# Kernel tuning notes

Measured on AMD Instinct MI355X. Metric: run time of the kernel, lower is better.

Reference implementation:

```python
import jax, jax.numpy as jnp
import numpy as np

N, E, NF, EF = 50000, 1600000, 16, 8
H, HEADS, HD, L = 128, 4, 32, 3
EPS = 1e-5
NEG_SLOPE = 0.2


def layer_norm(x, g, b):
    mu = jnp.mean(x, axis=-1, keepdims=True)
    var = jnp.mean((x - mu) ** 2, axis=-1, keepdims=True)
    return g * (x - mu) * jax.lax.rsqrt(var + EPS) + b


def setup_inputs() -> dict:
    key = jax.random.key(0)
    ks = jax.random.split(key, 16)
    s = 0.02
    return {
        "x": jax.random.normal(ks[0], (N, NF), jnp.float32),
        "edge_index": jax.random.randint(ks[1], (2, E), 0, N, jnp.int32),
        "edge_attr": jax.random.normal(ks[2], (E, EF), jnp.float32),
        "Wn": jax.random.normal(ks[3], (NF, H), jnp.float32) * s,
        "bn": jnp.zeros((H,), jnp.float32),
        "We": jax.random.normal(ks[4], (EF, H), jnp.float32) * s,
        "be": jnp.zeros((H,), jnp.float32),
        "ln_g": jnp.ones((L, H), jnp.float32),
        "ln_b": jnp.zeros((L, H), jnp.float32),
        "Wg": jax.random.normal(ks[5], (L, H, HEADS * HD), jnp.float32) * s,
        "att_s": jax.random.normal(ks[6], (L, HEADS, HD), jnp.float32) * s,
        "att_d": jax.random.normal(ks[7], (L, HEADS, HD), jnp.float32) * s,
        "att_e": jax.random.normal(ks[8], (L, HEADS, HD), jnp.float32) * s,
        "W_edge": jax.random.normal(ks[9], (L, H, HEADS * HD), jnp.float32) * s,
        "bg": jnp.zeros((L, HEADS * HD), jnp.float32),
    }


def reference(x, edge_index, edge_attr, Wn, bn, We, be, ln_g, ln_b, Wg, att_s, att_d, att_e, W_edge, bg):
    n = x.shape[0]
    h = x @ Wn + bn                      # [N, H] node embedding
    e = edge_attr @ We + be              # [E, H] edge embedding
    src, dst = edge_index[0], edge_index[1]
    # PyG add_self_loops(fill_value='mean'): self-loop attr = mean of incoming edge attrs
    cnt = jax.ops.segment_sum(jnp.ones((e.shape[0],), e.dtype), dst, num_segments=n)
    loop_attr = jax.ops.segment_sum(e, dst, num_segments=n) / jnp.maximum(cnt, 1.0)[:, None]
    ar = jnp.arange(n, dtype=src.dtype)
    src_f = jnp.concatenate([src, ar])   # [E+N]
    dst_f = jnp.concatenate([dst, ar])
    e_f = jnp.concatenate([e, loop_attr], axis=0)  # [E+N, H]
    for i in range(Wg.shape[0]):
        x_in = layer_norm(h, ln_g[i], ln_b[i])               # pre-norm
        xs = (x_in @ Wg[i]).reshape(n, HEADS, HD)            # [N, heads, hd]
        ep = (e_f @ W_edge[i]).reshape(-1, HEADS, HD)        # [E+N, heads, hd]
        a_src = jnp.sum(xs * att_s[i], axis=-1)              # [N, heads]
        a_dst = jnp.sum(xs * att_d[i], axis=-1)
        a_edge = jnp.sum(ep * att_e[i], axis=-1)             # [E+N, heads]
        alpha = jax.nn.leaky_relu(a_src[src_f] + a_dst[dst_f] + a_edge, NEG_SLOPE)
        # scatter-softmax over edges sharing a destination node
        alpha = alpha - jax.ops.segment_max(alpha, dst_f, num_segments=n)[dst_f]
        ex = jnp.exp(alpha)
        w = ex / jax.ops.segment_sum(ex, dst_f, num_segments=n)[dst_f]  # [E+N, heads]
        msg = w[:, :, None] * xs[src_f]                      # [E+N, heads, hd]
        out = jax.ops.segment_sum(msg, dst_f, num_segments=n).reshape(n, HEADS * HD) + bg[i]
        h = h + jax.nn.relu(out)                             # proj is Identity; dropout eval-mode
    graph_emb = jnp.mean(h, axis=0, keepdims=True)           # batch=None path
    return h, graph_emb
```

## Files before the change

### kernel.cpp

```cpp
#include <hip/hip_runtime.h>

#define NN 50000
#define EE 1600000
#define HC 128
#define EPSV 1e-5f
#define NEGS 0.2f

#define NB_H0 6250
#define NB_HIST 6250
#define NB_PREP 230

typedef __bf16 bf16x8 __attribute__((ext_vector_type(8)));
typedef __bf16 bf16x2 __attribute__((ext_vector_type(2)));
typedef float f32x4 __attribute__((ext_vector_type(4)));

static inline int cdiv(int a, int b) { return (a + b - 1) / b; }

__device__ inline float blo(unsigned v) { return __uint_as_float(v << 16); }
__device__ inline float bhi(unsigned v) { return __uint_as_float(v & 0xffff0000u); }
__device__ inline unsigned pkbf(float a, float b) {
  bf16x2 p;
  p.x = (__bf16)a;
  p.y = (__bf16)b;
  return *reinterpret_cast<unsigned*>(&p);
}

__global__ __launch_bounds__(256) void k_pre(const float* __restrict__ x, const float* __restrict__ Wn,
                                             const float* __restrict__ bn, const float* __restrict__ lng,
                                             const float* __restrict__ lnb, float* __restrict__ h,
                                             __bf16* __restrict__ xln, const int* __restrict__ ei,
                                             int* __restrict__ cnt, const float* __restrict__ We,
                                             const float* __restrict__ be, const float* __restrict__ Wed,
                                             const float* __restrict__ atte, float* __restrict__ Pc,
                                             const float* __restrict__ Wg, const float* __restrict__ atts,
                                             const float* __restrict__ attd, __bf16* __restrict__ wgt,
                                             int nb_hist) {
  int b = blockIdx.x;
  int t = threadIdx.x;
  if (b < NB_H0) {
    int idx = b * 256 + t;
    int n = idx >> 5, c4 = (idx & 31) * 4;
    float4 acc = *(const float4*)(bn + c4);
    const float* xr = x + (size_t)n * 16;
#pragma unroll
    for (int f = 0; f < 16; ++f) {
      float xv = xr[f];
      float4 wv = *(const float4*)(Wn + (size_t)f * HC + c4);
      acc.x += xv * wv.x;
      acc.y += xv * wv.y;
      acc.z += xv * wv.z;
      acc.w += xv * wv.w;
    }
    *(float4*)(h + (size_t)n * HC + c4) = acc;
    float s = acc.x + acc.y + acc.z + acc.w;
    float sq = acc.x * acc.x + acc.y * acc.y + acc.z * acc.z + acc.w * acc.w;
#pragma unroll
    for (int m = 1; m < 32; m <<= 1) {
      s += __shfl_xor(s, m);
      sq += __shfl_xor(sq, m);
    }
    float mu = s * (1.f / 128.f);
    float var = sq * (1.f / 128.f) - mu * mu;
    float rs = rsqrtf(fmaxf(var, 0.f) + EPSV);
    float4 g = *(const float4*)(lng + c4);
    float4 bb = *(const float4*)(lnb + c4);
    uint2 o;
    o.x = pkbf((acc.x - mu) * rs * g.x + bb.x, (acc.y - mu) * rs * g.y + bb.y);
    o.y = pkbf((acc.z - mu) * rs * g.z + bb.z, (acc.w - mu) * rs * g.w + bb.w);
    *(uint2*)(xln + (size_t)n * HC + c4) = o;
  } else if (b < NB_H0 + nb_hist) {
    int e = (b - NB_H0) * 256 + t;
    if (e < EE) atomicAdd(&cnt[ei[EE + e]], 1);
  } else if (b == NB_H0 + nb_hist) {
    __shared__ float v[128][4];
    for (int i = 0; i < 3; ++i) {
      if (t < 128) {
#pragma unroll
        for (int hh = 0; hh < 4; ++hh) {
          float s = 0.f;
          for (int hd = 0; hd < 32; ++hd)
            s += Wed[((size_t)i * 128 + t) * 128 + hh * 32 + hd] * atte[i * 128 + hh * 32 + hd];
          v[t][hh] = s;
        }
      }
      __syncthreads();
      if (t < 32) {
        int f = t >> 2, hh = t & 3;
        float s = 0.f;
        for (int c2 = 0; c2 < 128; ++c2) s += We[f * 128 + c2] * v[c2][hh];
        Pc[i * 36 + f * 4 + hh] = s;
      }
      if (t < 4) {
        float s = 0.f;
        for (int c2 = 0; c2 < 128; ++c2) s += be[c2] * v[c2][t];
        Pc[i * 36 + 32 + t] = s;
      }
      __syncthreads();
    }
  } else {
    int idx = (b - NB_H0 - nb_hist - 1) * 256 + t;
    if (idx >= 3 * 144 * 136) return;
    int i = idx / (144 * 136);
    int rem = idx - i * (144 * 136);
    int n = rem / 136, kp = rem - n * 136;
    float v = 0.f;
    if (kp < 128) {
      if (n < 128) {
        v = Wg[(size_t)i * 16384 + kp * 128 + n];
      } else if (n < 136) {
        int hh = (n - 128) & 3;
        const float* av = ((n < 132) ? atts : attd) + i * 128 + hh * 32;
        const float* wr = Wg + (size_t)i * 16384 + kp * 128 + hh * 32;
        float s = 0.f;
#pragma unroll
        for (int j = 0; j < 32; ++j) s += wr[j] * av[j];
        v = s;
      }
    }
    wgt[idx] = (__bf16)v;
  }
}

__global__ __launch_bounds__(1024) void k_scan1(const int* __restrict__ cnt, int* __restrict__ tmp,
                                                int* __restrict__ bsum) {
  __shared__ int lds[1024];
  int t = threadIdx.x;
  int i = blockIdx.x * 1024 + t;
  int v = (i < NN) ? cnt[i] : 0;
  lds[t] = v;
  __syncthreads();
  for (int off = 1; off < 1024; off <<= 1) {
    int u = (t >= off) ? lds[t - off] : 0;
    __syncthreads();
    lds[t] += u;
    __syncthreads();
  }
  if (i < NN) tmp[i] = lds[t] - v;
  if (t == 1023) bsum[blockIdx.x] = lds[1023];
}

__global__ void k_scan2(int* bsum, int nb) {
  if (threadIdx.x == 0 && blockIdx.x == 0) {
    int run = 0;
    for (int b = 0; b < nb; ++b) { int q = bsum[b]; bsum[b] = run; run += q; }
  }
}

__global__ __launch_bounds__(1024) void k_scan3(const int* __restrict__ tmp, const int* __restrict__ bsum,
                                                int* __restrict__ row_ptr, int* __restrict__ wr_ptr) {
  int t = threadIdx.x;
  int i = blockIdx.x * 1024 + t;
  if (i < NN) {
    int v = tmp[i] + bsum[blockIdx.x];
    row_ptr[i] = v;
    wr_ptr[i] = v;
  }
  if (i == 0) row_ptr[NN] = EE;
}

__global__ __launch_bounds__(256) void k_build(const int* __restrict__ ei, const float* __restrict__ ea,
                                               const float* __restrict__ Pc, int* __restrict__ cntr,
                                               uint4* __restrict__ rec, int cap) {
  __shared__ float P[108];
  if (threadIdx.x < 108) P[threadIdx.x] = Pc[threadIdx.x];
  __syncthreads();
  int e = blockIdx.x * 256 + threadIdx.x;
  if (e >= EE) return;
  int s = ei[e], d = ei[EE + e];
  const float* ar = ea + (size_t)e * 8;
  float4 q0 = *(const float4*)ar;
  float4 q1 = *(const float4*)(ar + 4);
  float a[8] = {q0.x, q0.y, q0.z, q0.w, q1.x, q1.y, q1.z, q1.w};
  float r[3][4];
#pragma unroll
  for (int i = 0; i < 3; ++i) {
    const float* p = P + i * 36;
#pragma unroll
    for (int hh = 0; hh < 4; ++hh) {
      float s2 = p[32 + hh];
#pragma unroll
      for (int f = 0; f < 8; ++f) s2 += a[f] * p[f * 4 + hh];
      r[i][hh] = s2;
    }
  }
  size_t idx;
  int pos = atomicAdd(&cntr[d], 1);
  if (cap == 0) {
    idx = (size_t)pos;
  } else {
    if (pos >= cap) return;
    idx = (size_t)d * cap + pos;
  }
  uint4 r0, r1;
  r0.x = (unsigned)s;
  r0.y = pkbf(r[0][0], r[0][1]);
  r0.z = pkbf(r[0][2], r[0][3]);
  r0.w = pkbf(r[1][0], r[1][1]);
  r1.x = pkbf(r[1][2], r[1][3]);
  r1.y = pkbf(r[2][0], r[2][1]);
  r1.z = pkbf(r[2][2], r[2][3]);
  r1.w = 0;
  uint4* rp = rec + idx * 2;
  rp[0] = r0;
  rp[1] = r1;
}

__global__ __launch_bounds__(256) void k_node(const __bf16* __restrict__ xln, const __bf16* __restrict__ wgt,
                                              __bf16* __restrict__ xsb, float* __restrict__ asrc,
                                              float* __restrict__ adst) {
  __shared__ __bf16 sA[128][136];
  __shared__ __bf16 sB[144][136];
  int t = threadIdx.x;
  int n0 = blockIdx.x * 128;
  {
    char* bd = (char*)&sB[0][0];
    const char* bs = (const char*)wgt;
    for (int off = t * 16; off < 144 * 136 * 2; off += 4096)
      *(uint4*)(bd + off) = *(const uint4*)(bs + off);
  }
  {
    uint4 z = make_uint4(0, 0, 0, 0);
#pragma unroll
    for (int u = t; u < 128 * 16; u += 256) {
      int row = u >> 4, ck = (u & 15) * 8;
      int n = n0 + row;
      uint4 v = (n < NN) ? *(const uint4*)(xln + (size_t)n * HC + ck) : z;
      *(uint4*)&sA[row][ck] = v;
    }
  }
  __syncthreads();
  int lane = t & 63;
  int c15 = lane & 15, g = lane >> 4;
  int m0w = (t >> 6) * 32;
  f32x4 acc[18];
#pragma unroll
  for (int i = 0; i < 18; ++i) acc[i] = (f32x4){0.f, 0.f, 0.f, 0.f};
#pragma unroll
  for (int ks = 0; ks < 4; ++ks) {
    bf16x8 a0 = *(const bf16x8*)&sA[m0w + c15][ks * 32 + g * 8];
    bf16x8 a1 = *(const bf16x8*)&sA[m0w + 16 + c15][ks * 32 + g * 8];
#pragma unroll
    for (int nt = 0; nt < 9; ++nt) {
      bf16x8 bv = *(const bf16x8*)&sB[nt * 16 + c15][ks * 32 + g * 8];
      acc[nt] = __builtin_amdgcn_mfma_f32_16x16x32_bf16(a0, bv, acc[nt], 0, 0, 0);
      acc[9 + nt] = __builtin_amdgcn_mfma_f32_16x16x32_bf16(a1, bv, acc[9 + nt], 0, 0, 0);
    }
  }
#pragma unroll
  for (int mt = 0; mt < 2; ++mt) {
    int nbase = n0 + m0w + mt * 16 + g * 4;
#pragma unroll
    for (int r = 0; r < 4; ++r) {
      int n = nbase + r;
      if (n < NN) {
        __bf16* op = xsb + (size_t)n * HC + c15;
#pragma unroll
        for (int nt = 0; nt < 8; ++nt) op[nt * 16] = (__bf16)acc[mt * 9 + nt][r];
        float av = acc[mt * 9 + 8][r];
        if (c15 < 4) asrc[(size_t)n * 4 + c15] = av;
        else if (c15 < 8) adst[(size_t)n * 4 + c15 - 4] = av;
      }
    }
  }
}

__global__ __launch_bounds__(256) void k_aggr(const int* __restrict__ row_ptr, const int* __restrict__ deg,
                                              int cap, const unsigned* __restrict__ recd, int loff,
                                              const __bf16* __restrict__ xsb, const float* __restrict__ asrc,
                                              const float* __restrict__ adst, const float* __restrict__ bgi,
                                              float* __restrict__ h, const float* __restrict__ lng2,
                                              const float* __restrict__ lnb2, __bf16* __restrict__ xln) {
  int wid = (blockIdx.x * 256 + threadIdx.x) >> 6;
  if (wid >= NN) return;
  int lane = threadIdx.x & 63;
  int ch0 = 2 * lane, head = lane >> 4;
  int um = lane & 7;
  int sbase = head << 4;
  int hs = head >> 1;
  int j0, j1;
  if (cap == 0) {
    j0 = row_ptr[wid];
    j1 = row_ptr[wid + 1];
  } else {
    j0 = wid * cap;
    int dg = deg[wid];
    if (dg > cap) dg = cap;
    j1 = j0 + dg;
  }
  float ad = adst[(size_t)wid * 4 + head];
  float acc0 = 0.f, acc1 = 0.f, dsum = 0.f, aes = 0.f;
  int nfull = (j1 - j0) >> 3;
  int j = j0 + nfull * 8;
  if (nfull > 0) {
    int ss[8], ssn[8];
#pragma unroll
    for (int u = 0; u < 8; ++u) ss[u] = (int)recd[(size_t)(j0 + u) * 8];
    for (int c = 0; c < nfull; ++c) {
      int jc = j0 + c * 8;
      if (c + 1 < nfull) {
#pragma unroll
        for (int u = 0; u < 8; ++u) ssn[u] = (int)recd[(size_t)(jc + 8 + u) * 8];
      } else {
#pragma unroll
        for (int u = 0; u < 8; ++u) ssn[u] = ss[u];
      }
      unsigned aw = recd[(size_t)(jc + um) * 8 + loff + hs];
      float av = (head & 1) ? bhi(aw) : blo(aw);
      float as = asrc[(size_t)ss[um] * 4 + head];
      unsigned xv[8];
#pragma unroll
      for (int u = 0; u < 8; ++u) xv[u] = *(const unsigned*)(xsb + (size_t)ss[u] * HC + ch0);
      float alpha = as + ad + av;
      alpha = alpha > 0.f ? alpha : NEGS * alpha;
      float em = __expf(alpha);
      aes += av;
#pragma unroll
      for (int u = 0; u < 8; ++u) {
        float e = __shfl(em, sbase + u);
        acc0 += e * blo(xv[u]);
        acc1 += e * bhi(xv[u]);
        dsum += e;
      }
#pragma unroll
      for (int u = 0; u < 8; ++u) ss[u] = ssn[u];
    }
  }
  aes += __shfl_xor(aes, 1);
  aes += __shfl_xor(aes, 2);
  aes += __shfl_xor(aes, 4);
  for (; j < j1; ++j) {
    const unsigned* rp = recd + (size_t)j * 8;
    int s0 = (int)rp[0];
    unsigned aw = rp[loff + hs];
    float v0 = (head & 1) ? bhi(aw) : blo(aw);
    float as0 = asrc[(size_t)s0 * 4 + head];
    unsigned x0 = *(const unsigned*)(xsb + (size_t)s0 * HC + ch0);
    float a0 = as0 + ad + v0;
    a0 = a0 > 0.f ? a0 : NEGS * a0;
    float e0 = __expf(a0);
    acc0 += e0 * blo(x0);
    acc1 += e0 * bhi(x0);
    dsum += e0;
    aes += v0;
  }
  int dg = j1 - j0;
  float aself = (dg > 0) ? aes / (float)dg : 0.f;
  float al = asrc[(size_t)wid * 4 + head] + ad + aself;
  al = al > 0.f ? al : NEGS * al;
  float exl = __expf(al);
  unsigned xv = *(const unsigned*)(xsb + (size_t)wid * HC + ch0);
  float inv = 1.f / (dsum + exl);
  float o0 = (acc0 + exl * blo(xv)) * inv;
  float o1 = (acc1 + exl * bhi(xv)) * inv;
  float* hp = h + (size_t)wid * HC;
  float n0v = hp[ch0] + fmaxf(0.f, o0 + bgi[ch0]);
  float n1v = hp[ch0 + 1] + fmaxf(0.f, o1 + bgi[ch0 + 1]);
  hp[ch0] = n0v;
  hp[ch0 + 1] = n1v;
  if (xln) {
    float s = n0v + n1v, sq = n0v * n0v + n1v * n1v;
#pragma unroll
    for (int m = 1; m < 64; m <<= 1) {
      s += __shfl_xor(s, m);
      sq += __shfl_xor(sq, m);
    }
    float mu = s * (1.f / 128.f);
    float var = sq * (1.f / 128.f) - mu * mu;
    float rs = rsqrtf(fmaxf(var, 0.f) + EPSV);
    unsigned p = pkbf((n0v - mu) * rs * lng2[ch0] + lnb2[ch0], (n1v - mu) * rs * lng2[ch0 + 1] + lnb2[ch0 + 1]);
    *(unsigned*)(xln + (size_t)wid * HC + ch0) = p;
  }
}

__global__ __launch_bounds__(256) void k_emb(const float* __restrict__ h, float* __restrict__ emb) {
  int t = blockIdx.x * 256 + threadIdx.x;
  int stride = gridDim.x * 256;
  float s = 0.f;
  for (int i = t; i < NN * HC; i += stride) s += h[i];
  __shared__ float red[256];
  red[threadIdx.x] = s;
  __syncthreads();
  if (threadIdx.x < 128) {
    float v2 = red[threadIdx.x] + red[threadIdx.x + 128];
    atomicAdd(&emb[threadIdx.x], v2 * (1.f / NN));
  }
}

extern "C" void kernel_launch(void* const* d_in, const int* in_sizes, int n_in, void* d_out, int out_size,
                              void* d_ws, size_t ws_size, hipStream_t stream) {
  (void)in_sizes; (void)n_in; (void)out_size;
  const float* x = (const float*)d_in[0];
  const int* ei = (const int*)d_in[1];
  const float* ea = (const float*)d_in[2];
  const float* Wn = (const float*)d_in[3];
  const float* bn = (const float*)d_in[4];
  const float* We = (const float*)d_in[5];
  const float* be = (const float*)d_in[6];
  const float* lng = (const float*)d_in[7];
  const float* lnb = (const float*)d_in[8];
  const float* Wg = (const float*)d_in[9];
  const float* atts = (const float*)d_in[10];
  const float* attd = (const float*)d_in[11];
  const float* atte = (const float*)d_in[12];
  const float* Wed = (const float*)d_in[13];
  const float* bg = (const float*)d_in[14];
  float* h = (float*)d_out;
  float* emb = h + (size_t)NN * HC;

  char* w = (char*)d_ws;
  size_t off = 0;
  auto alloc = [&](size_t bytes) {
    void* p = w + off;
    off = (off + bytes + 255) & ~(size_t)255;
    return p;
  };
  __bf16* xsb = (__bf16*)alloc((size_t)NN * HC * 2);
  __bf16* xln = (__bf16*)alloc((size_t)NN * HC * 2);
  float* asrc = (float*)alloc((size_t)NN * 4 * 4);
  float* adst = (float*)alloc((size_t)NN * 4 * 4);
  int* cnt = (int*)alloc((size_t)NN * 4);
  int* row_ptr = (int*)alloc((size_t)(NN + 1) * 4);
  int* wr_ptr = (int*)alloc((size_t)NN * 4);
  int* bsum = (int*)alloc(256);
  int* stmp = (int*)alloc((size_t)NN * 4);
  float* Pc = (float*)alloc(3 * 36 * 4);
  __bf16* wgt = (__bf16*)alloc((size_t)3 * 144 * 136 * 2);

  size_t avail = (ws_size > off + 4096) ? (ws_size - off - 4096) : 0;
  size_t capv = avail / ((size_t)NN * 32);
  int cap = 0;
  if (capv >= 72) cap = (capv > 96) ? 96 : (int)capv;
  uint4* rec = (uint4*)alloc(cap ? (size_t)NN * cap * 32 : (size_t)EE * 32);

  hipMemsetAsync(cnt, 0, (size_t)NN * 4, stream);
  hipMemsetAsync(emb, 0, HC * 4, stream);

  if (cap) {
    k_pre<<<NB_H0 + 1 + NB_PREP, 256, 0, stream>>>(x, Wn, bn, lng, lnb, h, xln, ei, cnt, We, be, Wed, atte,
                                                   Pc, Wg, atts, attd, wgt, 0);
    k_build<<<cdiv(EE, 256), 256, 0, stream>>>(ei, ea, Pc, cnt, rec, cap);
  } else {
    k_pre<<<NB_H0 + NB_HIST + 1 + NB_PREP, 256, 0, stream>>>(x, Wn, bn, lng, lnb, h, xln, ei, cnt, We, be,
                                                             Wed, atte, Pc, Wg, atts, attd, wgt, NB_HIST);
    int nb = cdiv(NN, 1024);
    k_scan1<<<nb, 1024, 0, stream>>>(cnt, stmp, bsum);
    k_scan2<<<1, 64, 0, stream>>>(bsum, nb);
    k_scan3<<<nb, 1024, 0, stream>>>(stmp, bsum, row_ptr, wr_ptr);
    k_build<<<cdiv(EE, 256), 256, 0, stream>>>(ei, ea, Pc, wr_ptr, rec, 0);
  }

  for (int i = 0; i < 3; ++i) {
    k_node<<<cdiv(NN, 128), 256, 0, stream>>>(xln, wgt + (size_t)i * 144 * 136, xsb, asrc, adst);
    const float* g2 = (i < 2) ? (lng + (i + 1) * HC) : nullptr;
    const float* b2 = (i < 2) ? (lnb + (i + 1) * HC) : nullptr;
    __bf16* xo = (i < 2) ? xln : nullptr;
    k_aggr<<<cdiv(NN, 4), 256, 0, stream>>>(row_ptr, cnt, cap, (const unsigned*)rec, 1 + 2 * i, xsb, asrc,
                                            adst, bg + i * HC, h, g2, b2, xo);
  }
  k_emb<<<512, 256, 0, stream>>>(h, emb);
}
```

Before: 433.0 us.

## Pack edge records to 16 bytes with FP8 logits and split wave across edges

Edge attention logits are now stored as software-encoded e4m3 bytes, so each edge record shrinks from 32 to 16 bytes. This halves the record traffic in the build and aggregation kernels and allows a larger per-node capacity for the same workspace. The aggregation wave is remapped so each lane handles 4 channels, with the two wave halves processing alternate edges and combining their partial sums at the end. The cost is lower precision on the edge logit term and half-idle lanes in the remainder loop and epilogue.

```diff
diff --git a/kernel.cpp b/kernel.cpp
--- a/kernel.cpp
+++ b/kernel.cpp
@@ -23,6 +23,19 @@
   p.x = (__bf16)a;
   p.y = (__bf16)b;
   return *reinterpret_cast<unsigned*>(&p);
+}
+
+__device__ inline float dec_e4m3(unsigned u) {
+  unsigned bits = ((u & 0x80u) << 24) | ((u & 0x7Fu) << 20);
+  return __uint_as_float(bits) * 0x1p120f;
+}
+__device__ inline unsigned enc_e4m3(float v) {
+  unsigned b = __float_as_uint(v * 0x1p-120f);
+  unsigned mag = (b & 0x7fffffffu) + 0x00080000u;
+  return ((b >> 24) & 0x80u) | ((mag >> 20) & 0x7Fu);
+}
+__device__ inline unsigned enc4_e4m3(const float* r) {
+  return enc_e4m3(r[0]) | (enc_e4m3(r[1]) << 8) | (enc_e4m3(r[2]) << 16) | (enc_e4m3(r[3]) << 24);
 }
 
 __global__ __launch_bounds__(256) void k_pre(const float* __restrict__ x, const float* __restrict__ Wn,
@@ -160,7 +173,7 @@
 
 __global__ __launch_bounds__(256) void k_build(const int* __restrict__ ei, const float* __restrict__ ea,
                                                const float* __restrict__ Pc, int* __restrict__ cntr,
-                                               uint4* __restrict__ rec, int cap) {
+                                               unsigned char* __restrict__ rec8, int cap) {
   __shared__ float P[108];
   if (threadIdx.x < 108) P[threadIdx.x] = Pc[threadIdx.x];
   __syncthreads();
@@ -191,18 +204,12 @@
     if (pos >= cap) return;
     idx = (size_t)d * cap + pos;
   }
-  uint4 r0, r1;
-  r0.x = (unsigned)s;
-  r0.y = pkbf(r[0][0], r[0][1]);
-  r0.z = pkbf(r[0][2], r[0][3]);
-  r0.w = pkbf(r[1][0], r[1][1]);
-  r1.x = pkbf(r[1][2], r[1][3]);
-  r1.y = pkbf(r[2][0], r[2][1]);
-  r1.z = pkbf(r[2][2], r[2][3]);
-  r1.w = 0;
-  uint4* rp = rec + idx * 2;
-  rp[0] = r0;
-  rp[1] = r1;
+  uint4 rr;
+  rr.x = (unsigned)s;
+  rr.y = enc4_e4m3(r[0]);
+  rr.z = enc4_e4m3(r[1]);
+  rr.w = enc4_e4m3(r[2]);
+  *(uint4*)(rec8 + idx * 16) = rr;
 }
 
 __global__ __launch_bounds__(256) void k_node(const __bf16* __restrict__ xln, const __bf16* __restrict__ wgt,
@@ -265,7 +272,7 @@
 }
 
 __global__ __launch_bounds__(256) void k_aggr(const int* __restrict__ row_ptr, const int* __restrict__ deg,
-                                              int cap, const unsigned* __restrict__ recd, int loff,
+                                              int cap, const unsigned char* __restrict__ rec8, int layer,
                                               const __bf16* __restrict__ xsb, const float* __restrict__ asrc,
                                               const float* __restrict__ adst, const float* __restrict__ bgi,
                                               float* __restrict__ h, const float* __restrict__ lng2,
@@ -273,10 +280,10 @@
   int wid = (blockIdx.x * 256 + threadIdx.x) >> 6;
   if (wid >= NN) return;
   int lane = threadIdx.x & 63;
-  int ch0 = 2 * lane, head = lane >> 4;
-  int um = lane & 7;
-  int sbase = head << 4;
-  int hs = head >> 1;
+  int q = lane & 31, half = lane >> 5;
+  int ch0 = 4 * q, headc = q >> 3;
+  int um = lane & 7, headS = lane >> 4;
+  int aoff = 4 + 4 * layer + headS;
   int j0, j1;
   if (cap == 0) {
     j0 = row_ptr[wid];
@@ -287,38 +294,52 @@
     if (dg > cap) dg = cap;
     j1 = j0 + dg;
   }
-  float ad = adst[(size_t)wid * 4 + head];
-  float acc0 = 0.f, acc1 = 0.f, dsum = 0.f, aes = 0.f;
+  float adS = adst[(size_t)wid * 4 + headS];
+  float a0 = 0.f, a1 = 0.f, a2 = 0.f, a3 = 0.f, dsum = 0.f, aes = 0.f;
   int nfull = (j1 - j0) >> 3;
   int j = j0 + nfull * 8;
   if (nfull > 0) {
     int ss[8], ssn[8];
 #pragma unroll
-    for (int u = 0; u < 8; ++u) ss[u] = (int)recd[(size_t)(j0 + u) * 8];
+    for (int u = 0; u < 8; ++u) ss[u] = *(const int*)(rec8 + (size_t)(j0 + u) * 16);
     for (int c = 0; c < nfull; ++c) {
       int jc = j0 + c * 8;
       if (c + 1 < nfull) {
 #pragma unroll
-        for (int u = 0; u < 8; ++u) ssn[u] = (int)recd[(size_t)(jc + 8 + u) * 8];
+        for (int u = 0; u < 8; ++u) ssn[u] = *(const int*)(rec8 + (size_t)(jc + 8 + u) * 16);
       } else {
 #pragma unroll
         for (int u = 0; u < 8; ++u) ssn[u] = ss[u];
       }
-      unsigned aw = recd[(size_t)(jc + um) * 8 + loff + hs];
-      float av = (head & 1) ? bhi(aw) : blo(aw);
-      float as = asrc[(size_t)ss[um] * 4 + head];
-      unsigned xv[8];
-#pragma unroll
-      for (int u = 0; u < 8; ++u) xv[u] = *(const unsigned*)(xsb + (size_t)ss[u] * HC + ch0);
-      float alpha = as + ad + av;
+      float av = dec_e4m3(rec8[(size_t)(jc + um) * 16 + aoff]);
+      float as = asrc[(size_t)ss[um] * 4 + headS];
+      uint2 g0 = *(const uint2*)(xsb + (size_t)ss[0 + half] * HC + ch0);
+      uint2 g1 = *(const uint2*)(xsb + (size_t)ss[2 + half] * HC + ch0);
+      uint2 g2 = *(const uint2*)(xsb + (size_t)ss[4 + half] * HC + ch0);
+      uint2 g3 = *(const uint2*)(xsb + (size_t)ss[6 + half] * HC + ch0);
+      float alpha = as + adS + av;
       alpha = alpha > 0.f ? alpha : NEGS * alpha;
       float em = __expf(alpha);
       aes += av;
-#pragma unroll
-      for (int u = 0; u < 8; ++u) {
-        float e = __shfl(em, sbase + u);
-        acc0 += e * blo(xv[u]);
-        acc1 += e * bhi(xv[u]);
+      int sb = headc << 4;
+      {
+        float e = __shfl(em, sb + 0 + half);
+        a0 += e * blo(g0.x); a1 += e * bhi(g0.x); a2 += e * blo(g0.y); a3 += e * bhi(g0.y);
+        dsum += e;
+      }
+      {
+        float e = __shfl(em, sb + 2 + half);
+        a0 += e * blo(g1.x); a1 += e * bhi(g1.x); a2 += e * blo(g1.y); a3 += e * bhi(g1.y);
+        dsum += e;
+      }
+      {
+        float e = __shfl(em, sb + 4 + half);
+        a0 += e * blo(g2.x); a1 += e * bhi(g2.x); a2 += e * blo(g2.y); a3 += e * bhi(g2.y);
+        dsum += e;
+      }
+      {
+        float e = __shfl(em, sb + 6 + half);
+        a0 += e * blo(g3.x); a1 += e * bhi(g3.x); a2 += e * blo(g3.y); a3 += e * bhi(g3.y);
         dsum += e;
       }
 #pragma unroll
@@ -329,46 +350,63 @@
   aes += __shfl_xor(aes, 2);
   aes += __shfl_xor(aes, 4);
   for (; j < j1; ++j) {
-    const unsigned* rp = recd + (size_t)j * 8;
-    int s0 = (int)rp[0];
-    unsigned aw = rp[loff + hs];
-    float v0 = (head & 1) ? bhi(aw) : blo(aw);
-    float as0 = asrc[(size_t)s0 * 4 + head];
-    unsigned x0 = *(const unsigned*)(xsb + (size_t)s0 * HC + ch0);
-    float a0 = as0 + ad + v0;
-    a0 = a0 > 0.f ? a0 : NEGS * a0;
-    float e0 = __expf(a0);
-    acc0 += e0 * blo(x0);
-    acc1 += e0 * bhi(x0);
-    dsum += e0;
-    aes += v0;
-  }
+    int s0 = *(const int*)(rec8 + (size_t)j * 16);
+    float v0s = dec_e4m3(rec8[(size_t)j * 16 + aoff]);
+    float as0 = asrc[(size_t)s0 * 4 + headS];
+    float al0 = as0 + adS + v0s;
+    al0 = al0 > 0.f ? al0 : NEGS * al0;
+    float e0 = __expf(al0);
+    aes += v0s;
+    float ec = __shfl(e0, headc << 4);
+    if (half == 0) {
+      uint2 g = *(const uint2*)(xsb + (size_t)s0 * HC + ch0);
+      a0 += ec * blo(g.x); a1 += ec * bhi(g.x); a2 += ec * blo(g.y); a3 += ec * bhi(g.y);
+      dsum += ec;
+    }
+  }
+  a0 += __shfl_xor(a0, 32);
+  a1 += __shfl_xor(a1, 32);
+  a2 += __shfl_xor(a2, 32);
+  a3 += __shfl_xor(a3, 32);
+  dsum += __shfl_xor(dsum, 32);
+  float aesC = __shfl(aes, headc << 4);
   int dg = j1 - j0;
-  float aself = (dg > 0) ? aes / (float)dg : 0.f;
-  float al = asrc[(size_t)wid * 4 + head] + ad + aself;
+  float aself = (dg > 0) ? aesC / (float)dg : 0.f;
+  float al = asrc[(size_t)wid * 4 + headc] + adst[(size_t)wid * 4 + headc] + aself;
   al = al > 0.f ? al : NEGS * al;
   float exl = __expf(al);
-  unsigned xv = *(const unsigned*)(xsb + (size_t)wid * HC + ch0);
+  uint2 gs = *(const uint2*)(xsb + (size_t)wid * HC + ch0);
   float inv = 1.f / (dsum + exl);
-  float o0 = (acc0 + exl * blo(xv)) * inv;
-  float o1 = (acc1 + exl * bhi(xv)) * inv;
-  float* hp = h + (size_t)wid * HC;
-  float n0v = hp[ch0] + fmaxf(0.f, o0 + bgi[ch0]);
-  float n1v = hp[ch0 + 1] + fmaxf(0.f, o1 + bgi[ch0 + 1]);
-  hp[ch0] = n0v;
-  hp[ch0 + 1] = n1v;
-  if (xln) {
-    float s = n0v + n1v, sq = n0v * n0v + n1v * n1v;
-#pragma unroll
-    for (int m = 1; m < 64; m <<= 1) {
-      s += __shfl_xor(s, m);
-      sq += __shfl_xor(sq, m);
-    }
-    float mu = s * (1.f / 128.f);
-    float var = sq * (1.f / 128.f) - mu * mu;
-    float rs = rsqrtf(fmaxf(var, 0.f) + EPSV);
-    unsigned p = pkbf((n0v - mu) * rs * lng2[ch0] + lnb2[ch0], (n1v - mu) * rs * lng2[ch0 + 1] + lnb2[ch0 + 1]);
-    *(unsigned*)(xln + (size_t)wid * HC + ch0) = p;
+  float o0 = (a0 + exl * blo(gs.x)) * inv;
+  float o1 = (a1 + exl * bhi(gs.x)) * inv;
+  float o2 = (a2 + exl * blo(gs.y)) * inv;
+  float o3 = (a3 + exl * bhi(gs.y)) * inv;
+  if (half == 0) {
+    float4 hv = *(float4*)(h + (size_t)wid * HC + ch0);
+    float4 bgv = *(const float4*)(bgi + ch0);
+    float n0v = hv.x + fmaxf(0.f, o0 + bgv.x);
+    float n1v = hv.y + fmaxf(0.f, o1 + bgv.y);
+    float n2v = hv.z + fmaxf(0.f, o2 + bgv.z);
+    float n3v = hv.w + fmaxf(0.f, o3 + bgv.w);
+    *(float4*)(h + (size_t)wid * HC + ch0) = make_float4(n0v, n1v, n2v, n3v);
+    if (xln) {
+      float s = n0v + n1v + n2v + n3v;
+      float sq = n0v * n0v + n1v * n1v + n2v * n2v + n3v * n3v;
+#pragma unroll
+      for (int m = 1; m < 32; m <<= 1) {
+        s += __shfl_xor(s, m);
+        sq += __shfl_xor(sq, m);
+      }
+      float mu = s * (1.f / 128.f);
+      float var = sq * (1.f / 128.f) - mu * mu;
+      float rs = rsqrtf(fmaxf(var, 0.f) + EPSV);
+      float4 g = *(const float4*)(lng2 + ch0);
+      float4 b = *(const float4*)(lnb2 + ch0);
+      uint2 o;
+      o.x = pkbf((n0v - mu) * rs * g.x + b.x, (n1v - mu) * rs * g.y + b.y);
+      o.y = pkbf((n2v - mu) * rs * g.z + b.z, (n3v - mu) * rs * g.w + b.w);
+      *(uint2*)(xln + (size_t)wid * HC + ch0) = o;
+    }
   }
 }
 
@@ -427,10 +465,10 @@
   __bf16* wgt = (__bf16*)alloc((size_t)3 * 144 * 136 * 2);
 
   size_t avail = (ws_size > off + 4096) ? (ws_size - off - 4096) : 0;
-  size_t capv = avail / ((size_t)NN * 32);
+  size_t capv = avail / ((size_t)NN * 16);
   int cap = 0;
   if (capv >= 72) cap = (capv > 96) ? 96 : (int)capv;
-  uint4* rec = (uint4*)alloc(cap ? (size_t)NN * cap * 32 : (size_t)EE * 32);
+  unsigned char* rec8 = (unsigned char*)alloc(cap ? (size_t)NN * cap * 16 : (size_t)EE * 16);
 
   hipMemsetAsync(cnt, 0, (size_t)NN * 4, stream);
   hipMemsetAsync(emb, 0, HC * 4, stream);
@@ -438,7 +476,7 @@
   if (cap) {
     k_pre<<<NB_H0 + 1 + NB_PREP, 256, 0, stream>>>(x, Wn, bn, lng, lnb, h, xln, ei, cnt, We, be, Wed, atte,
                                                    Pc, Wg, atts, attd, wgt, 0);
-    k_build<<<cdiv(EE, 256), 256, 0, stream>>>(ei, ea, Pc, cnt, rec, cap);
+    k_build<<<cdiv(EE, 256), 256, 0, stream>>>(ei, ea, Pc, cnt, rec8, cap);
   } else {
     k_pre<<<NB_H0 + NB_HIST + 1 + NB_PREP, 256, 0, stream>>>(x, Wn, bn, lng, lnb, h, xln, ei, cnt, We, be,
                                                              Wed, atte, Pc, Wg, atts, attd, wgt, NB_HIST);
@@ -446,7 +484,7 @@
     k_scan1<<<nb, 1024, 0, stream>>>(cnt, stmp, bsum);
     k_scan2<<<1, 64, 0, stream>>>(bsum, nb);
     k_scan3<<<nb, 1024, 0, stream>>>(stmp, bsum, row_ptr, wr_ptr);
-    k_build<<<cdiv(EE, 256), 256, 0, stream>>>(ei, ea, Pc, wr_ptr, rec, 0);
+    k_build<<<cdiv(EE, 256), 256, 0, stream>>>(ei, ea, Pc, wr_ptr, rec8, 0);
   }
 
   for (int i = 0; i < 3; ++i) {
@@ -454,8 +492,8 @@
     const float* g2 = (i < 2) ? (lng + (i + 1) * HC) : nullptr;
     const float* b2 = (i < 2) ? (lnb + (i + 1) * HC) : nullptr;
     __bf16* xo = (i < 2) ? xln : nullptr;
-    k_aggr<<<cdiv(NN, 4), 256, 0, stream>>>(row_ptr, cnt, cap, (const unsigned*)rec, 1 + 2 * i, xsb, asrc,
-                                            adst, bg + i * HC, h, g2, b2, xo);
+    k_aggr<<<cdiv(NN, 4), 256, 0, stream>>>(row_ptr, cnt, cap, rec8, i, xsb, asrc, adst, bg + i * HC, h,
+                                            g2, b2, xo);
   }
   k_emb<<<512, 256, 0, stream>>>(h, emb);
 }
```

New measurement: 494.1 us. 1.14x slower.
